# Optimization experiments

Measured on AMD Instinct MI355X. Metric: run time of the kernel, lower is better.

The kernel has to match this reference:

```python
import jax, jax.numpy as jnp
import numpy as np

B, N, IN_DIM, OUT_DIM = 8, 2048, 128, 128
NEG_SLOPE = 0.2

def setup_inputs() -> dict:
    key = jax.random.key(0)
    k1, k2, k3, k4 = jax.random.split(key, 4)
    x = jax.random.normal(k1, (B, N, IN_DIM), dtype=jnp.float32)
    adj = jax.random.randint(k2, (N, N), 0, 2, dtype=jnp.int32)
    # nn.Linear weight init scale ~ 1/sqrt(fan_in)
    W = jax.random.normal(k3, (IN_DIM, OUT_DIM), dtype=jnp.float32) / np.sqrt(IN_DIM)
    a_vec = jax.random.normal(k4, (2 * OUT_DIM,), dtype=jnp.float32) / np.sqrt(2 * OUT_DIM)
    return {"x": x, "adj": adj, "W": W, "a_vec": a_vec}

def reference(x, adj, W, a_vec):
    # h = x @ W : [b, n, d]
    h = jnp.einsum("bni,io->bno", x, W)
    # Algebraic decomposition of a([h_i, h_j]) = a1.h_i + a2.h_j
    a1, a2 = a_vec[:OUT_DIM], a_vec[OUT_DIM:]
    s_i = h @ a1  # [b, n] score contribution from source node i
    s_j = h @ a2  # [b, n] score contribution from target node j
    e = s_i[:, :, None] + s_j[:, None, :]  # [b, n, n]
    e = jnp.where(e >= 0, e, NEG_SLOPE * e)  # leaky_relu(0.2)
    mask = (adj > 0)[None, :, :]  # [1, n, n] broadcast over batch
    e = jnp.where(mask, e, -jnp.inf)
    alpha = jax.nn.softmax(e, axis=-1)  # [b, n, n]
    out = jnp.einsum("bnm,bmd->bnd", alpha, h)  # [b, n, d]
    return out, alpha
```

## Files before the change

kernel.cpp:

```cpp
#include <hip/hip_runtime.h>
#include <hip/hip_bf16.h>
#include <cstdint>
#include <cstddef>

constexpr int Bn = 8;
constexpr int Nn = 2048;
constexpr int Dn = 128;

typedef __bf16 bf16x8 __attribute__((ext_vector_type(8)));
typedef float f32x4 __attribute__((ext_vector_type(4)));

#define AS1 __attribute__((address_space(1)))
#define AS3 __attribute__((address_space(3)))

static __device__ __forceinline__ void gl_lds16(const void* g, void* l) {
  __builtin_amdgcn_global_load_lds((AS1 const void*)g, (AS3 void*)l, 16, 0, 0);
}

__global__ __launch_bounds__(256) void gat_k1(
    const float* __restrict__ x, const float* __restrict__ W,
    const float* __restrict__ a_vec,
    __bf16* __restrict__ hT, float* __restrict__ s1, float* __restrict__ s2) {
  __shared__ __align__(16) float Wl[64 * 144];
  __shared__ __align__(16) float xL[32 * 132];

  const int t = threadIdx.x;
  const int r0 = blockIdx.x * 32;
  const int b = r0 >> 11;
  const int n0 = r0 & (Nn - 1);
  const int rp = (t >> 4) << 1;
  const int c0 = (t & 15) << 3;
  const int c0p = c0 + ((c0 >> 5) << 2);

  float acc[2][8];
#pragma unroll
  for (int r = 0; r < 2; ++r)
#pragma unroll
    for (int c = 0; c < 8; ++c) acc[r][c] = 0.f;

#pragma unroll
  for (int it = 0; it < 4; ++it) {
    int idx = t + (it << 8);
    int rr = idx >> 5, kc = (idx & 31) << 2;
    *(float4*)(xL + rr * 132 + kc) = *(const float4*)(x + (size_t)(r0 + rr) * Dn + kc);
  }

  for (int ph = 0; ph < 2; ++ph) {
    if (ph) __syncthreads();
#pragma unroll
    for (int it = 0; it < 8; ++it) {
      int idx = t + (it << 8);
      int kk = idx >> 5, c4 = (idx & 31) << 2;
      int dsto = kk * 144 + c4 + ((c4 >> 5) << 2);
      *(float4*)(Wl + dsto) = *(const float4*)(W + (size_t)((ph << 6) + kk) * Dn + c4);
    }
    __syncthreads();
    const float* xrow = xL + rp * 132 + (ph << 6);
    for (int k = 0; k < 64; ++k) {
      float xa0 = xrow[k];
      float xa1 = xrow[132 + k];
      float4 w0 = *(const float4*)(Wl + k * 144 + c0p);
      float4 w1 = *(const float4*)(Wl + k * 144 + c0p + 4);
      float ws[8] = {w0.x, w0.y, w0.z, w0.w, w1.x, w1.y, w1.z, w1.w};
#pragma unroll
      for (int c = 0; c < 8; ++c) {
        acc[0][c] = fmaf(xa0, ws[c], acc[0][c]);
        acc[1][c] = fmaf(xa1, ws[c], acc[1][c]);
      }
    }
  }

  float q1[2] = {0.f, 0.f}, q2[2] = {0.f, 0.f};
#pragma unroll
  for (int c = 0; c < 8; ++c) {
    float a1c = a_vec[c0 + c];
    float a2c = a_vec[Dn + c0 + c];
    q1[0] = fmaf(acc[0][c], a1c, q1[0]);
    q1[1] = fmaf(acc[1][c], a1c, q1[1]);
    q2[0] = fmaf(acc[0][c], a2c, q2[0]);
    q2[1] = fmaf(acc[1][c], a2c, q2[1]);
  }
#pragma unroll
  for (int d = 1; d < 16; d <<= 1) {
    q1[0] += __shfl_xor(q1[0], d);
    q1[1] += __shfl_xor(q1[1], d);
    q2[0] += __shfl_xor(q2[0], d);
    q2[1] += __shfl_xor(q2[1], d);
  }
  if ((t & 15) == 0) {
    s1[b * Nn + n0 + rp] = q1[0];
    s1[b * Nn + n0 + rp + 1] = q1[1];
    s2[b * Nn + n0 + rp] = q2[0];
    s2[b * Nn + n0 + rp + 1] = q2[1];
  }

#pragma unroll
  for (int c = 0; c < 8; ++c) {
    union { __bf16 h[2]; uint32_t u; } pk;
    pk.h[0] = (__bf16)acc[0][c];
    pk.h[1] = (__bf16)acc[1][c];
    *(uint32_t*)(hT + (size_t)(b * Dn + c0 + c) * Nn + n0 + rp) = pk.u;
  }
}

__global__ __launch_bounds__(512) void gat_k2(
    const int* __restrict__ adj, const __bf16* __restrict__ hT,
    const float* __restrict__ s1, const float* __restrict__ s2,
    float* __restrict__ out, float* __restrict__ alpha) {
  __shared__ __align__(16) float sj[Nn];
  __shared__ float siv[32], invl[32];
  __shared__ __align__(16) __bf16 Pl[2][32 * 72];
  __shared__ __align__(16) __bf16 hl[2][128 * 64];

  const int t = threadIdx.x;
  const int b = blockIdx.x >> 6;
  const int i0 = (blockIdx.x & 63) << 5;
  const int w = t >> 6, lane = t & 63;
  const int ii = t >> 4, sub = t & 15;
  const int lrow = lane >> 3, ccs = lane & 7;
  const __bf16* __restrict__ hTb = hT + (size_t)b * Dn * Nn;

#pragma unroll
  for (int inst = 0; inst < 2; ++inst) {
    int row = (w << 4) + (inst << 3) + lrow;
    gl_lds16(hTb + (size_t)row * Nn + ((ccs ^ lrow) << 3),
             &hl[0][((w << 4) + (inst << 3)) << 6]);
  }

  *(float4*)(sj + (t << 2)) = *(const float4*)(s2 + b * Nn + (t << 2));
  if (t < 32) siv[t] = s1[b * Nn + i0 + t];
  __syncthreads();

  const int i = i0 + ii;
  const int* __restrict__ adjrow = adj + (size_t)i * Nn;
  const float si = siv[ii];

  float l = 0.f;
  for (int cc = 0; cc < 32; ++cc) {
    int j = (cc << 6) + (sub << 2);
    int4 am = *(const int4*)(adjrow + j);
    float4 sv = *(const float4*)(sj + j);
    float e;
    e = si + sv.x; e = fmaxf(e, 0.2f * e); l += (am.x > 0) ? __expf(e) : 0.f;
    e = si + sv.y; e = fmaxf(e, 0.2f * e); l += (am.y > 0) ? __expf(e) : 0.f;
    e = si + sv.z; e = fmaxf(e, 0.2f * e); l += (am.z > 0) ? __expf(e) : 0.f;
    e = si + sv.w; e = fmaxf(e, 0.2f * e); l += (am.w > 0) ? __expf(e) : 0.f;
  }
  l += __shfl_xor(l, 1);
  l += __shfl_xor(l, 2);
  l += __shfl_xor(l, 4);
  l += __shfl_xor(l, 8);
  if (sub == 0) invl[ii] = 1.f / l;
  __syncthreads();
  const float il = invl[ii];

  const int iw = (w & 1) << 4;
  const int nd0 = (w >> 1) << 5;
  const int q16 = lane >> 4, m16 = lane & 15;
  f32x4 acc0 = {0.f, 0.f, 0.f, 0.f}, acc1 = {0.f, 0.f, 0.f, 0.f};
  float* __restrict__ arow = alpha + ((size_t)(b * Nn + i) << 11);

  for (int jt = 0; jt < 32; ++jt) {
    const int buf = jt & 1;
    const int j0 = jt << 6;
    {
      int j = j0 + (sub << 2);
      int4 am = *(const int4*)(adjrow + j);
      float4 sv = *(const float4*)(sj + j);
      float e0 = si + sv.x; e0 = fmaxf(e0, 0.2f * e0);
      float e1 = si + sv.y; e1 = fmaxf(e1, 0.2f * e1);
      float e2 = si + sv.z; e2 = fmaxf(e2, 0.2f * e2);
      float e3 = si + sv.w; e3 = fmaxf(e3, 0.2f * e3);
      float a0 = (am.x > 0) ? __expf(e0) * il : 0.f;
      float a1 = (am.y > 0) ? __expf(e1) * il : 0.f;
      float a2 = (am.z > 0) ? __expf(e2) * il : 0.f;
      float a3 = (am.w > 0) ? __expf(e3) * il : 0.f;
      *(float4*)(arow + j) = make_float4(a0, a1, a2, a3);
      union { __bf16 h[4]; uint2 u; } pk;
      pk.h[0] = (__bf16)a0; pk.h[1] = (__bf16)a1;
      pk.h[2] = (__bf16)a2; pk.h[3] = (__bf16)a3;
      *(uint2*)(&Pl[buf][ii * 72 + (sub << 2)]) = pk.u;
    }
    __syncthreads();
    if (jt < 31) {
      int jn = j0 + 64;
#pragma unroll
      for (int inst = 0; inst < 2; ++inst) {
        int row = (w << 4) + (inst << 3) + lrow;
        gl_lds16(hTb + (size_t)row * Nn + jn + ((ccs ^ lrow) << 3),
                 &hl[buf ^ 1][((w << 4) + (inst << 3)) << 6]);
      }
    }
#pragma unroll
    for (int ks = 0; ks < 2; ++ks) {
      bf16x8 af = *(const bf16x8*)(&Pl[buf][(iw + m16) * 72 + (ks << 5) + (q16 << 3)]);
      {
        int d = nd0 + m16;
        int phys = ((ks << 2) + q16) ^ (d & 7);
        bf16x8 bv = *(const bf16x8*)(&hl[buf][(d << 6) + (phys << 3)]);
        acc0 = __builtin_amdgcn_mfma_f32_16x16x32_bf16(af, bv, acc0, 0, 0, 0);
      }
      {
        int d = nd0 + 16 + m16;
        int phys = ((ks << 2) + q16) ^ (d & 7);
        bf16x8 bv = *(const bf16x8*)(&hl[buf][(d << 6) + (phys << 3)]);
        acc1 = __builtin_amdgcn_mfma_f32_16x16x32_bf16(af, bv, acc1, 0, 0, 0);
      }
    }
  }

#pragma unroll
  for (int nb = 0; nb < 2; ++nb) {
    f32x4 a = nb ? acc1 : acc0;
    int d = nd0 + (nb << 4) + m16;
#pragma unroll
    for (int r = 0; r < 4; ++r) {
      int irow = i0 + iw + (q16 << 2) + r;
      out[((size_t)(b * Nn + irow) << 7) + d] = a[r];
    }
  }
}

extern "C" void kernel_launch(void* const* d_in, const int* in_sizes, int n_in,
                              void* d_out, int out_size, void* d_ws, size_t ws_size,
                              hipStream_t stream) {
  const float* x = (const float*)d_in[0];
  const int* adj = (const int*)d_in[1];
  const float* W = (const float*)d_in[2];
  const float* a_vec = (const float*)d_in[3];

  float* out = (float*)d_out;
  float* alpha = out + (size_t)Bn * Nn * Dn;

  char* ws = (char*)d_ws;
  __bf16* hT = (__bf16*)ws;
  float* s1 = (float*)(ws + (size_t)Bn * Dn * Nn * 2);
  float* s2 = s1 + (size_t)Bn * Nn;

  gat_k1<<<512, 256, 0, stream>>>(x, W, a_vec, hT, s1, s2);
  gat_k2<<<512, 512, 0, stream>>>(adj, hT, s1, s2, out, alpha);
}
```

Measured before the change: 195.2 us.

## Defer softmax normalization to epilogue and stream alpha writes after matmul

Removes the separate row-sum pass before the P@h loop. The main loop now accumulates unnormalized exp weights into the MFMA and sums the row total on the fly, prefetching the next adj/sj tile into registers. The output is scaled by 1/l in the epilogue, and alpha is written in a second pass over adj with nontemporal stores. The adj reads stay at two passes and exp is still computed twice. Using unnormalized bf16 P values can change rounding and risks overflow if scores are large.

Result: slower. 213.2 us (+9.2%).

```diff
diff --git a/kernel.cpp b/kernel.cpp
--- a/kernel.cpp
+++ b/kernel.cpp
@@ -135,61 +135,43 @@
   const int* __restrict__ adjrow = adj + (size_t)i * Nn;
   const float si = siv[ii];
 
-  float l = 0.f;
-  for (int cc = 0; cc < 32; ++cc) {
-    int j = (cc << 6) + (sub << 2);
-    int4 am = *(const int4*)(adjrow + j);
-    float4 sv = *(const float4*)(sj + j);
-    float e;
-    e = si + sv.x; e = fmaxf(e, 0.2f * e); l += (am.x > 0) ? __expf(e) : 0.f;
-    e = si + sv.y; e = fmaxf(e, 0.2f * e); l += (am.y > 0) ? __expf(e) : 0.f;
-    e = si + sv.z; e = fmaxf(e, 0.2f * e); l += (am.z > 0) ? __expf(e) : 0.f;
-    e = si + sv.w; e = fmaxf(e, 0.2f * e); l += (am.w > 0) ? __expf(e) : 0.f;
-  }
-  l += __shfl_xor(l, 1);
-  l += __shfl_xor(l, 2);
-  l += __shfl_xor(l, 4);
-  l += __shfl_xor(l, 8);
-  if (sub == 0) invl[ii] = 1.f / l;
-  __syncthreads();
-  const float il = invl[ii];
-
   const int iw = (w & 1) << 4;
   const int nd0 = (w >> 1) << 5;
   const int q16 = lane >> 4, m16 = lane & 15;
   f32x4 acc0 = {0.f, 0.f, 0.f, 0.f}, acc1 = {0.f, 0.f, 0.f, 0.f};
-  float* __restrict__ arow = alpha + ((size_t)(b * Nn + i) << 11);
+  float l = 0.f;
+
+  int4 am = *(const int4*)(adjrow + (sub << 2));
+  float4 sv = *(const float4*)(sj + (sub << 2));
 
   for (int jt = 0; jt < 32; ++jt) {
     const int buf = jt & 1;
-    const int j0 = jt << 6;
     {
-      int j = j0 + (sub << 2);
-      int4 am = *(const int4*)(adjrow + j);
-      float4 sv = *(const float4*)(sj + j);
       float e0 = si + sv.x; e0 = fmaxf(e0, 0.2f * e0);
       float e1 = si + sv.y; e1 = fmaxf(e1, 0.2f * e1);
       float e2 = si + sv.z; e2 = fmaxf(e2, 0.2f * e2);
       float e3 = si + sv.w; e3 = fmaxf(e3, 0.2f * e3);
-      float a0 = (am.x > 0) ? __expf(e0) * il : 0.f;
-      float a1 = (am.y > 0) ? __expf(e1) * il : 0.f;
-      float a2 = (am.z > 0) ? __expf(e2) * il : 0.f;
-      float a3 = (am.w > 0) ? __expf(e3) * il : 0.f;
-      *(float4*)(arow + j) = make_float4(a0, a1, a2, a3);
+      float p0 = (am.x > 0) ? __expf(e0) : 0.f;
+      float p1 = (am.y > 0) ? __expf(e1) : 0.f;
+      float p2 = (am.z > 0) ? __expf(e2) : 0.f;
+      float p3 = (am.w > 0) ? __expf(e3) : 0.f;
+      l += p0; l += p1; l += p2; l += p3;
       union { __bf16 h[4]; uint2 u; } pk;
-      pk.h[0] = (__bf16)a0; pk.h[1] = (__bf16)a1;
-      pk.h[2] = (__bf16)a2; pk.h[3] = (__bf16)a3;
+      pk.h[0] = (__bf16)p0; pk.h[1] = (__bf16)p1;
+      pk.h[2] = (__bf16)p2; pk.h[3] = (__bf16)p3;
       *(uint2*)(&Pl[buf][ii * 72 + (sub << 2)]) = pk.u;
     }
     __syncthreads();
     if (jt < 31) {
-      int jn = j0 + 64;
+      int jn = (jt + 1) << 6;
 #pragma unroll
       for (int inst = 0; inst < 2; ++inst) {
         int row = (w << 4) + (inst << 3) + lrow;
         gl_lds16(hTb + (size_t)row * Nn + jn + ((ccs ^ lrow) << 3),
                  &hl[buf ^ 1][((w << 4) + (inst << 3)) << 6]);
       }
+      am = *(const int4*)(adjrow + jn + (sub << 2));
+      sv = *(const float4*)(sj + jn + (sub << 2));
     }
 #pragma unroll
     for (int ks = 0; ks < 2; ++ks) {
@@ -209,6 +191,16 @@
     }
   }
 
+  l += __shfl_xor(l, 1);
+  l += __shfl_xor(l, 2);
+  l += __shfl_xor(l, 4);
+  l += __shfl_xor(l, 8);
+  if (sub == 0) invl[ii] = 1.f / l;
+  __syncthreads();
+
+  float ils[4];
+#pragma unroll
+  for (int r = 0; r < 4; ++r) ils[r] = invl[iw + (q16 << 2) + r];
 #pragma unroll
   for (int nb = 0; nb < 2; ++nb) {
     f32x4 a = nb ? acc1 : acc0;
@@ -216,8 +208,28 @@
 #pragma unroll
     for (int r = 0; r < 4; ++r) {
       int irow = i0 + iw + (q16 << 2) + r;
-      out[((size_t)(b * Nn + irow) << 7) + d] = a[r];
-    }
+      __builtin_nontemporal_store(a[r] * ils[r],
+                                  &out[((size_t)(b * Nn + irow) << 7) + d]);
+    }
+  }
+
+  const float il = invl[ii];
+  float* __restrict__ arow = alpha + ((size_t)(b * Nn + i) << 11);
+#pragma unroll 2
+  for (int jt = 0; jt < 32; ++jt) {
+    int j = (jt << 6) + (sub << 2);
+    int4 am2 = *(const int4*)(adjrow + j);
+    float4 sv2 = *(const float4*)(sj + j);
+    float e0 = si + sv2.x; e0 = fmaxf(e0, 0.2f * e0);
+    float e1 = si + sv2.y; e1 = fmaxf(e1, 0.2f * e1);
+    float e2 = si + sv2.z; e2 = fmaxf(e2, 0.2f * e2);
+    float e3 = si + sv2.w; e3 = fmaxf(e3, 0.2f * e3);
+    float a0 = (am2.x > 0) ? __expf(e0) * il : 0.f;
+    float a1 = (am2.y > 0) ? __expf(e1) * il : 0.f;
+    float a2 = (am2.z > 0) ? __expf(e2) * il : 0.f;
+    float a3 = (am2.w > 0) ? __expf(e3) * il : 0.f;
+    f32x4 av = {a0, a1, a2, a3};
+    __builtin_nontemporal_store(av, (f32x4*)(arow + j));
   }
 }
 
```

## Cache adjacency mask as bitmasks, use nontemporal alpha stores and lighter barrier

Applied to the files above, without the earlier changes.

The first softmax pass now records the adjacency mask as per-thread bitmasks in registers, so the second pass no longer re-reads adj from global memory. Alpha stores become nontemporal to avoid polluting cache. The loop is restructured into 4 groups of 8 unrolled tiles, with a custom waitcnt+barrier that lets the alpha store stay in flight. This adds register pressure and relies on precise vmcnt accounting for correctness.

After: 192.8 us. About the same (-1.2%).

```diff
diff --git a/kernel.cpp b/kernel.cpp
--- a/kernel.cpp
+++ b/kernel.cpp
@@ -136,16 +136,33 @@
   const float si = siv[ii];
 
   float l = 0.f;
-  for (int cc = 0; cc < 32; ++cc) {
-    int j = (cc << 6) + (sub << 2);
-    int4 am = *(const int4*)(adjrow + j);
-    float4 sv = *(const float4*)(sj + j);
-    float e;
-    e = si + sv.x; e = fmaxf(e, 0.2f * e); l += (am.x > 0) ? __expf(e) : 0.f;
-    e = si + sv.y; e = fmaxf(e, 0.2f * e); l += (am.y > 0) ? __expf(e) : 0.f;
-    e = si + sv.z; e = fmaxf(e, 0.2f * e); l += (am.z > 0) ? __expf(e) : 0.f;
-    e = si + sv.w; e = fmaxf(e, 0.2f * e); l += (am.w > 0) ? __expf(e) : 0.f;
-  }
+  uint32_t mb0 = 0, mb1 = 0, mb2 = 0, mb3 = 0;
+#define PASS1_G(G, MW)                                                        \
+  {                                                                           \
+    _Pragma("unroll")                                                         \
+    for (int u = 0; u < 8; ++u) {                                             \
+      int j = (((G) << 3) + u) * 64 + (sub << 2);                             \
+      int4 am = *(const int4*)(adjrow + j);                                   \
+      float4 sv = *(const float4*)(sj + j);                                   \
+      float e0 = si + sv.x; e0 = fmaxf(e0, 0.2f * e0);                        \
+      float e1 = si + sv.y; e1 = fmaxf(e1, 0.2f * e1);                        \
+      float e2 = si + sv.z; e2 = fmaxf(e2, 0.2f * e2);                        \
+      float e3 = si + sv.w; e3 = fmaxf(e3, 0.2f * e3);                        \
+      l += (am.x > 0) ? __expf(e0) : 0.f;                                     \
+      l += (am.y > 0) ? __expf(e1) : 0.f;                                     \
+      l += (am.z > 0) ? __expf(e2) : 0.f;                                     \
+      l += (am.w > 0) ? __expf(e3) : 0.f;                                     \
+      uint32_t mbt = (am.x > 0 ? 1u : 0u) | (am.y > 0 ? 2u : 0u) |            \
+                     (am.z > 0 ? 4u : 0u) | (am.w > 0 ? 8u : 0u);             \
+      MW |= mbt << (u << 2);                                                  \
+    }                                                                         \
+  }
+  PASS1_G(0, mb0)
+  PASS1_G(1, mb1)
+  PASS1_G(2, mb2)
+  PASS1_G(3, mb3)
+#undef PASS1_G
+
   l += __shfl_xor(l, 1);
   l += __shfl_xor(l, 2);
   l += __shfl_xor(l, 4);
@@ -160,51 +177,56 @@
   f32x4 acc0 = {0.f, 0.f, 0.f, 0.f}, acc1 = {0.f, 0.f, 0.f, 0.f};
   float* __restrict__ arow = alpha + ((size_t)(b * Nn + i) << 11);
 
-  for (int jt = 0; jt < 32; ++jt) {
-    const int buf = jt & 1;
-    const int j0 = jt << 6;
-    {
-      int j = j0 + (sub << 2);
-      int4 am = *(const int4*)(adjrow + j);
-      float4 sv = *(const float4*)(sj + j);
-      float e0 = si + sv.x; e0 = fmaxf(e0, 0.2f * e0);
-      float e1 = si + sv.y; e1 = fmaxf(e1, 0.2f * e1);
-      float e2 = si + sv.z; e2 = fmaxf(e2, 0.2f * e2);
-      float e3 = si + sv.w; e3 = fmaxf(e3, 0.2f * e3);
-      float a0 = (am.x > 0) ? __expf(e0) * il : 0.f;
-      float a1 = (am.y > 0) ? __expf(e1) * il : 0.f;
-      float a2 = (am.z > 0) ? __expf(e2) * il : 0.f;
-      float a3 = (am.w > 0) ? __expf(e3) * il : 0.f;
-      *(float4*)(arow + j) = make_float4(a0, a1, a2, a3);
-      union { __bf16 h[4]; uint2 u; } pk;
-      pk.h[0] = (__bf16)a0; pk.h[1] = (__bf16)a1;
-      pk.h[2] = (__bf16)a2; pk.h[3] = (__bf16)a3;
-      *(uint2*)(&Pl[buf][ii * 72 + (sub << 2)]) = pk.u;
-    }
-    __syncthreads();
-    if (jt < 31) {
-      int jn = j0 + 64;
-#pragma unroll
-      for (int inst = 0; inst < 2; ++inst) {
-        int row = (w << 4) + (inst << 3) + lrow;
-        gl_lds16(hTb + (size_t)row * Nn + jn + ((ccs ^ lrow) << 3),
-                 &hl[buf ^ 1][((w << 4) + (inst << 3)) << 6]);
-      }
-    }
-#pragma unroll
-    for (int ks = 0; ks < 2; ++ks) {
-      bf16x8 af = *(const bf16x8*)(&Pl[buf][(iw + m16) * 72 + (ks << 5) + (q16 << 3)]);
+  for (int g = 0; g < 4; ++g) {
+    const uint32_t mw = (g & 2) ? ((g & 1) ? mb3 : mb2) : ((g & 1) ? mb1 : mb0);
+#pragma unroll
+    for (int u = 0; u < 8; ++u) {
+      const int buf = u & 1;
+      const int j0r = (g << 9) + (u << 6);
       {
-        int d = nd0 + m16;
-        int phys = ((ks << 2) + q16) ^ (d & 7);
-        bf16x8 bv = *(const bf16x8*)(&hl[buf][(d << 6) + (phys << 3)]);
-        acc0 = __builtin_amdgcn_mfma_f32_16x16x32_bf16(af, bv, acc0, 0, 0, 0);
-      }
-      {
-        int d = nd0 + 16 + m16;
-        int phys = ((ks << 2) + q16) ^ (d & 7);
-        bf16x8 bv = *(const bf16x8*)(&hl[buf][(d << 6) + (phys << 3)]);
-        acc1 = __builtin_amdgcn_mfma_f32_16x16x32_bf16(af, bv, acc1, 0, 0, 0);
+        int j = j0r + (sub << 2);
+        float4 sv = *(const float4*)(sj + j);
+        float e0 = si + sv.x; e0 = fmaxf(e0, 0.2f * e0);
+        float e1 = si + sv.y; e1 = fmaxf(e1, 0.2f * e1);
+        float e2 = si + sv.z; e2 = fmaxf(e2, 0.2f * e2);
+        float e3 = si + sv.w; e3 = fmaxf(e3, 0.2f * e3);
+        float a0 = (mw & (1u << ((u << 2) + 0))) ? __expf(e0) * il : 0.f;
+        float a1 = (mw & (1u << ((u << 2) + 1))) ? __expf(e1) * il : 0.f;
+        float a2 = (mw & (1u << ((u << 2) + 2))) ? __expf(e2) * il : 0.f;
+        float a3 = (mw & (1u << ((u << 2) + 3))) ? __expf(e3) * il : 0.f;
+        f32x4 av = {a0, a1, a2, a3};
+        __builtin_nontemporal_store(av, (f32x4*)(arow + j));
+        union { __bf16 h[4]; uint2 u2; } pk;
+        pk.h[0] = (__bf16)a0; pk.h[1] = (__bf16)a1;
+        pk.h[2] = (__bf16)a2; pk.h[3] = (__bf16)a3;
+        *(uint2*)(&Pl[buf][ii * 72 + (sub << 2)]) = pk.u2;
+      }
+      asm volatile("s_waitcnt vmcnt(1) lgkmcnt(0)\n\ts_barrier" ::: "memory");
+      if (u < 7 || g < 3) {
+        int jn = j0r + 64;
+#pragma unroll
+        for (int inst = 0; inst < 2; ++inst) {
+          int row = (w << 4) + (inst << 3) + lrow;
+          gl_lds16(hTb + (size_t)row * Nn + jn + ((ccs ^ lrow) << 3),
+                   &hl[buf ^ 1][((w << 4) + (inst << 3)) << 6]);
+        }
+      }
+      __builtin_amdgcn_sched_barrier(0);
+#pragma unroll
+      for (int ks = 0; ks < 2; ++ks) {
+        bf16x8 af = *(const bf16x8*)(&Pl[buf][(iw + m16) * 72 + (ks << 5) + (q16 << 3)]);
+        {
+          int d = nd0 + m16;
+          int phys = ((ks << 2) + q16) ^ (d & 7);
+          bf16x8 bv = *(const bf16x8*)(&hl[buf][(d << 6) + (phys << 3)]);
+          acc0 = __builtin_amdgcn_mfma_f32_16x16x32_bf16(af, bv, acc0, 0, 0, 0);
+        }
+        {
+          int d = nd0 + 16 + m16;
+          int phys = ((ks << 2) + q16) ^ (d & 7);
+          bf16x8 bv = *(const bf16x8*)(&hl[buf][(d << 6) + (phys << 3)]);
+          acc1 = __builtin_amdgcn_mfma_f32_16x16x32_bf16(af, bv, acc1, 0, 0, 0);
+        }
       }
     }
   }
```
